# Kernel tuning notes

Measured on AMD Instinct MI355X. Metric: run time of the kernel, lower is better.

Reference implementation:

```python
import jax, jax.numpy as jnp
import numpy as np

NUM_CONCEPT = 256
NUM_QUESTION = 10000
DIM_EMB = 64
TIME_LOG = 5.0
BATCH, SEQ = 32, 1024


def setup_inputs() -> dict:
    key = jax.random.key(0)
    ks = jax.random.split(key, 10)
    concept_seq = jax.random.randint(ks[0], (BATCH, SEQ), 0, NUM_CONCEPT)
    question_seq = jax.random.randint(ks[1], (BATCH, SEQ), 0, NUM_QUESTION)
    correctness_seq = jax.random.randint(ks[2], (BATCH, SEQ), 0, 2)
    time_seq = jnp.sort(jax.random.randint(ks[3], (BATCH, SEQ), 0, 1000000), axis=-1)
    std = 0.01  # nn.init.normal_(..., std=0.01)
    alpha_inter_emb = std * jax.random.normal(ks[4], (2 * NUM_CONCEPT, DIM_EMB), jnp.float32)
    alpha_concept_emb = std * jax.random.normal(ks[5], (NUM_CONCEPT, DIM_EMB), jnp.float32)
    beta_inter_emb = std * jax.random.normal(ks[6], (2 * NUM_CONCEPT, DIM_EMB), jnp.float32)
    beta_concept_emb = std * jax.random.normal(ks[7], (NUM_CONCEPT, DIM_EMB), jnp.float32)
    question_bias = std * jax.random.normal(ks[8], (NUM_QUESTION, 1), jnp.float32)
    concept_bias = std * jax.random.normal(ks[9], (NUM_CONCEPT, 1), jnp.float32)
    return {
        "concept_seq": concept_seq,
        "question_seq": question_seq,
        "correctness_seq": correctness_seq,
        "time_seq": time_seq,
        "alpha_inter_emb": alpha_inter_emb,
        "alpha_concept_emb": alpha_concept_emb,
        "beta_inter_emb": beta_inter_emb,
        "beta_concept_emb": beta_concept_emb,
        "question_bias": question_bias,
        "concept_bias": concept_bias,
    }


def reference(concept_seq, question_seq, correctness_seq, time_seq,
              alpha_inter_emb, alpha_concept_emb, beta_inter_emb,
              beta_concept_emb, question_bias, concept_bias):
    num_concept = alpha_concept_emb.shape[0]
    seq_len = concept_seq.shape[1]
    inters = concept_seq + correctness_seq * num_concept  # [B,S]

    # small batched matmuls producing [B,S,S]
    alphas = jnp.einsum("bid,bjd->bij", alpha_inter_emb[inters], alpha_concept_emb[concept_seq])
    betas = jnp.clip(jnp.einsum("bid,bjd->bij", beta_inter_emb[inters], beta_concept_emb[concept_seq]) + 1.0, 0.0, 10.0)

    t = time_seq.astype(jnp.float32)
    delta_t = jnp.abs(t[:, :, None] - t[:, None, :])  # [B,S,S]
    delta_t = jnp.log(delta_t + 1e-10) / np.log(TIME_LOG).astype(np.float32)

    cross_effects = alphas * jnp.exp(-betas * delta_t)

    # keep strictly upper triangle (source i strictly before target j), sum over sources
    causal = jnp.triu(jnp.ones((seq_len, seq_len), jnp.float32), k=1)
    sum_t = jnp.sum(cross_effects * causal[None], axis=-2)  # [B,S]

    problem_bias = question_bias[question_seq][..., 0]
    skill_bias = concept_bias[concept_seq][..., 0]
    predict_score_batch = jax.nn.sigmoid(problem_bias + skill_bias + sum_t)[:, 1:]
    return predict_score_batch
```

## Files before the change

kernel.cpp:

```cpp
#include <hip/hip_runtime.h>
#include <hip/hip_bf16.h>
#include <math.h>

#define SEQ     1024
#define NBATCH  32
#define NC      256
#define NI      512
#define DIM     64
#define JT      64
#define NJT     (SEQ / JT)
#define NWAVE   16

__global__ __launch_bounds__(256) void build_tables(
    const float* __restrict__ aI, const float* __restrict__ aC,
    const float* __restrict__ bI, const float* __restrict__ bC,
    __hip_bfloat162* __restrict__ tab)
{
    __shared__ float sA[DIM];
    __shared__ float sB[DIM];
    const int x = blockIdx.x;
    const int t = threadIdx.x;
    if (t < DIM)            sA[t]        = aI[x * DIM + t];
    else if (t < 2 * DIM)   sB[t - DIM]  = bI[x * DIM + (t - DIM)];
    __syncthreads();

    const int y = t;
    const float4* ca = (const float4*)(aC + y * DIM);
    const float4* cb = (const float4*)(bC + y * DIM);
    float da = 0.f, db = 0.f;
#pragma unroll
    for (int k = 0; k < DIM / 4; ++k) {
        float4 va = ca[k];
        float4 vb = cb[k];
        da += sA[4*k+0]*va.x + sA[4*k+1]*va.y + sA[4*k+2]*va.z + sA[4*k+3]*va.w;
        db += sB[4*k+0]*vb.x + sB[4*k+1]*vb.y + sB[4*k+2]*vb.z + sB[4*k+3]*vb.w;
    }
    const float inv_ln5 = 0.6213349345596119f;
    float beta = fminf(fmaxf(db + 1.0f, 0.0f), 10.0f) * inv_ln5;
    __hip_bfloat162 v;
    v.x = __float2bfloat16(da);
    v.y = __float2bfloat16(beta);
    tab[x * NC + y] = v;
}

__global__ __launch_bounds__(1024) void hawkes_main(
    const int* __restrict__ concept_seq, const int* __restrict__ question_seq,
    const int* __restrict__ correct_seq, const int* __restrict__ time_seq,
    const __hip_bfloat162* __restrict__ tab,
    const float* __restrict__ qbias, const float* __restrict__ cbias,
    float* __restrict__ out)
{
    __shared__ float2 st[SEQ];
    __shared__ float  part[NWAVE][2][JT];

    const int b   = blockIdx.x;
    const int p   = blockIdx.y;
    const int tid = threadIdx.x;
    const int w   = tid >> 6;
    const int l   = tid & 63;

    const int jtB = (NJT - 1) - p;
    const int jtS = p;
    const int I_B = (jtB + 1) * JT;
    const int I_S = (jtS + 1) * JT;

    if (tid < I_B) {
        int c   = concept_seq[b * SEQ + tid];
        int off = (c + (correct_seq[b * SEQ + tid] << 8)) << 10;
        st[tid] = make_float2(__int_as_float(off), (float)time_seq[b * SEQ + tid]);
    }
    __syncthreads();

    const int   jB   = jtB * JT + l;
    const int   jS   = jtS * JT + l;
    const int   cB4  = concept_seq[b * SEQ + jB] * 4;
    const int   cS4  = concept_seq[b * SEQ + jS] * 4;
    const float tjB  = st[jB].y;
    const float tjS  = st[jS].y;

    const char* tabc = (const char*)tab;
    float accB = 0.0f, accS = 0.0f;

    const int nks = I_S >> 4;
    const int nkb = I_B >> 4;

#pragma unroll 4
    for (int k = 0; k < nks; ++k) {
        const int i = w + (k << 4);
        float2 sv = st[i];
        const char* row = tabc + __float_as_int(sv.x);
        unsigned uB = *(const unsigned*)(row + cB4);
        unsigned uS = *(const unsigned*)(row + cS4);
        float dlB = __builtin_amdgcn_logf(fabsf(tjB - sv.y) + 1e-10f);
        float dlS = __builtin_amdgcn_logf(fabsf(tjS - sv.y) + 1e-10f);
        float aB  = __uint_as_float(uB << 16);
        float bB  = __uint_as_float(uB & 0xFFFF0000u);
        float aS  = __uint_as_float(uS << 16);
        float bS  = __uint_as_float(uS & 0xFFFF0000u);
        float eB  = __builtin_amdgcn_exp2f(-bB * dlB);
        float eS  = __builtin_amdgcn_exp2f(-bS * dlS);
        accB += (i < jB) ? aB * eB : 0.0f;
        accS += (i < jS) ? aS * eS : 0.0f;
    }
#pragma unroll 4
    for (int k = nks; k < nkb; ++k) {
        const int i = w + (k << 4);
        float2 sv = st[i];
        unsigned uB = *(const unsigned*)(tabc + __float_as_int(sv.x) + cB4);
        float dlB = __builtin_amdgcn_logf(fabsf(tjB - sv.y) + 1e-10f);
        float aB  = __uint_as_float(uB << 16);
        float bB  = __uint_as_float(uB & 0xFFFF0000u);
        accB += (i < jB) ? aB * __builtin_amdgcn_exp2f(-bB * dlB) : 0.0f;
    }

    part[w][0][l] = accB;
    part[w][1][l] = accS;
    __syncthreads();

    if (w < 2) {
        const int j  = (w == 0) ? jB : jS;
        float s = 0.0f;
#pragma unroll
        for (int k = 0; k < NWAVE; ++k) s += part[k][w][l];
        if (j >= 1) {
            float zv = qbias[question_seq[b * SEQ + j]]
                     + cbias[concept_seq[b * SEQ + j]] + s;
            float ez = __builtin_amdgcn_exp2f(-zv * 1.4426950408889634f);
            out[b * (SEQ - 1) + (j - 1)] = 1.0f / (1.0f + ez);
        }
    }
}

extern "C" void kernel_launch(void* const* d_in, const int* in_sizes, int n_in,
                              void* d_out, int out_size, void* d_ws, size_t ws_size,
                              hipStream_t stream) {
    const int*   concept_seq  = (const int*)  d_in[0];
    const int*   question_seq = (const int*)  d_in[1];
    const int*   correct_seq  = (const int*)  d_in[2];
    const int*   time_seq     = (const int*)  d_in[3];
    const float* aI           = (const float*)d_in[4];
    const float* aC           = (const float*)d_in[5];
    const float* bI           = (const float*)d_in[6];
    const float* bC           = (const float*)d_in[7];
    const float* qbias        = (const float*)d_in[8];
    const float* cbias        = (const float*)d_in[9];
    float*       out          = (float*)d_out;

    __hip_bfloat162* tab = (__hip_bfloat162*)d_ws;

    build_tables<<<NI, 256, 0, stream>>>(aI, aC, bI, bC, tab);
    hawkes_main<<<dim3(NBATCH, NJT / 2), 1024, 0, stream>>>(
        concept_seq, question_seq, correct_seq, time_seq, tab, qbias, cbias, out);
}
```

Before: 100.4 us.

## Split source-index reduction across two blocks and finalize in separate kernel

Adds a z grid dimension of 2 so each (batch, tile-pair) block handles half of the source range, writing partial sums to workspace. A new finalize kernel adds the two partials, applies the biases and the sigmoid. This doubles the grid from 256 to 512 blocks to fill more CUs on the MI355X, at the cost of an extra kernel launch and a global round trip for the partial sums. It also sets a min-blocks hint in launch_bounds and changes the unroll factor.

```diff
diff --git a/kernel.cpp b/kernel.cpp
--- a/kernel.cpp
+++ b/kernel.cpp
@@ -10,6 +10,8 @@
 #define JT      64
 #define NJT     (SEQ / JT)
 #define NWAVE   16
+
+#define PART_OFF (NI * NC * 4)
 
 __global__ __launch_bounds__(256) void build_tables(
     const float* __restrict__ aI, const float* __restrict__ aC,
@@ -43,18 +45,18 @@
     tab[x * NC + y] = v;
 }
 
-__global__ __launch_bounds__(1024) void hawkes_main(
-    const int* __restrict__ concept_seq, const int* __restrict__ question_seq,
+__global__ __launch_bounds__(1024, 8) void hawkes_main(
+    const int* __restrict__ concept_seq,
     const int* __restrict__ correct_seq, const int* __restrict__ time_seq,
     const __hip_bfloat162* __restrict__ tab,
-    const float* __restrict__ qbias, const float* __restrict__ cbias,
-    float* __restrict__ out)
+    float* __restrict__ partial)
 {
     __shared__ float2 st[SEQ];
     __shared__ float  part[NWAVE][2][JT];
 
     const int b   = blockIdx.x;
     const int p   = blockIdx.y;
+    const int z   = blockIdx.z;
     const int tid = threadIdx.x;
     const int w   = tid >> 6;
     const int l   = tid & 63;
@@ -81,12 +83,11 @@
     const char* tabc = (const char*)tab;
     float accB = 0.0f, accS = 0.0f;
 
-    const int nks = I_S >> 4;
-    const int nkb = I_B >> 4;
-
-#pragma unroll 4
-    for (int k = 0; k < nks; ++k) {
-        const int i = w + (k << 4);
+    const int nksh  = I_S >> 5;
+    const int baseS = z * (I_S >> 1);
+#pragma unroll 2
+    for (int k = 0; k < nksh; ++k) {
+        const int i = baseS + w + (k << 4);
         float2 sv = st[i];
         const char* row = tabc + __float_as_int(sv.x);
         unsigned uB = *(const unsigned*)(row + cB4);
@@ -102,9 +103,11 @@
         accB += (i < jB) ? aB * eB : 0.0f;
         accS += (i < jS) ? aS * eS : 0.0f;
     }
+    const int nkbh  = (I_B - I_S) >> 5;
+    const int baseB = I_S + z * ((I_B - I_S) >> 1);
 #pragma unroll 4
-    for (int k = nks; k < nkb; ++k) {
-        const int i = w + (k << 4);
+    for (int k = 0; k < nkbh; ++k) {
+        const int i = baseB + w + (k << 4);
         float2 sv = st[i];
         unsigned uB = *(const unsigned*)(tabc + __float_as_int(sv.x) + cB4);
         float dlB = __builtin_amdgcn_logf(fabsf(tjB - sv.y) + 1e-10f);
@@ -118,17 +121,28 @@
     __syncthreads();
 
     if (w < 2) {
-        const int j  = (w == 0) ? jB : jS;
+        const int jt = (w == 0) ? jtB : jtS;
         float s = 0.0f;
 #pragma unroll
         for (int k = 0; k < NWAVE; ++k) s += part[k][w][l];
-        if (j >= 1) {
-            float zv = qbias[question_seq[b * SEQ + j]]
-                     + cbias[concept_seq[b * SEQ + j]] + s;
-            float ez = __builtin_amdgcn_exp2f(-zv * 1.4426950408889634f);
-            out[b * (SEQ - 1) + (j - 1)] = 1.0f / (1.0f + ez);
-        }
+        partial[((z * NBATCH + b) * NJT + jt) * JT + l] = s;
     }
+}
+
+__global__ __launch_bounds__(256) void finalize(
+    const float* __restrict__ partial,
+    const int* __restrict__ concept_seq, const int* __restrict__ question_seq,
+    const float* __restrict__ qbias, const float* __restrict__ cbias,
+    float* __restrict__ out)
+{
+    const int idx = blockIdx.x * 256 + threadIdx.x;
+    const int b = idx >> 10;
+    const int j = idx & (SEQ - 1);
+    if (j < 1) return;
+    float s = partial[b * SEQ + j] + partial[(NBATCH + b) * SEQ + j];
+    float zv = qbias[question_seq[b * SEQ + j]] + cbias[concept_seq[b * SEQ + j]] + s;
+    float ez = __builtin_amdgcn_exp2f(-zv * 1.4426950408889634f);
+    out[b * (SEQ - 1) + (j - 1)] = 1.0f / (1.0f + ez);
 }
 
 extern "C" void kernel_launch(void* const* d_in, const int* in_sizes, int n_in,
@@ -147,8 +161,11 @@
     float*       out          = (float*)d_out;
 
     __hip_bfloat162* tab = (__hip_bfloat162*)d_ws;
+    float* partial = (float*)((char*)d_ws + PART_OFF);
 
     build_tables<<<NI, 256, 0, stream>>>(aI, aC, bI, bC, tab);
-    hawkes_main<<<dim3(NBATCH, NJT / 2), 1024, 0, stream>>>(
-        concept_seq, question_seq, correct_seq, time_seq, tab, qbias, cbias, out);
+    hawkes_main<<<dim3(NBATCH, NJT / 2, 2), 1024, 0, stream>>>(
+        concept_seq, correct_seq, time_seq, tab, partial);
+    finalize<<<(NBATCH * SEQ) / 256, 256, 0, stream>>>(
+        partial, concept_seq, question_seq, qbias, cbias, out);
 }
```

Result: no change. 101.9 us (+1.5%).
